# Kernel tuning notes

Hardware: AMD Instinct MI355X
Metric: run time of the kernel (lower is better)

The kernel has to match this reference:

```python
import jax, jax.numpy as jnp
import numpy as np

B, T = 4, 512
V, D, L, H, F = 32000, 1024, 12, 16, 4096
HD = D // H
CUTS = [0, 2000, 8000, V]
SHRINK = 4


def layer_norm(x, s, b, eps=1e-5):
    m = jnp.mean(x, axis=-1, keepdims=True)
    v = jnp.var(x, axis=-1, keepdims=True)
    return (x - m) * jax.lax.rsqrt(v + eps) * s + b


def rel_shift(x):
    # Transformer-XL relative shift. x: [B, H, T, S] with S == T.
    b, h, t, s = x.shape
    x = jnp.pad(x, ((0, 0), (0, 0), (0, 0), (1, 0)))
    x = x.reshape(b, h, s + 1, t)[:, :, 1:, :]
    return x.reshape(b, h, t, s)


def sinusoid_pos_emb(seq_len, dim):
    # positions seq_len-1 ... 0 (TXL convention), [seq_len, dim]
    pos = jnp.arange(seq_len - 1, -1, -1.0, dtype=jnp.float32)
    inv_freq = 1.0 / (10000.0 ** (jnp.arange(0, dim, 2, dtype=jnp.float32) / dim))
    ang = pos[:, None] * inv_freq[None, :]
    return jnp.concatenate([jnp.sin(ang), jnp.cos(ang)], axis=-1)


def setup_inputs() -> dict:
    key = jax.random.key(0)
    ks = iter(jax.random.split(key, 64))

    def n(shape, std=0.02):
        return jax.random.normal(next(ks), shape, dtype=jnp.float32) * std

    hids = [D // (SHRINK ** i) for i in range(3)]  # 1024, 256, 64
    inp = {}
    inp['x'] = jax.random.randint(next(ks), (B, T), 0, V)
    inp['emb_0'] = n([CUTS[1] - CUTS[0], hids[0]])
    inp['emb_1'] = n([CUTS[2] - CUTS[1], hids[1]])
    inp['emb_2'] = n([CUTS[3] - CUTS[2], hids[2]])
    inp['proj_1'] = n([hids[1], D], 0.01)
    inp['proj_2'] = n([hids[2], D], 0.01)
    inp['out_bias'] = jnp.zeros([V], jnp.float32)
    inp['r_w_bias'] = n([1, 1, H, HD])
    inp['r_r_bias'] = n([1, 1, H, HD])
    inp['ln1_s'] = jnp.ones([L, D], jnp.float32)
    inp['ln1_b'] = jnp.zeros([L, D], jnp.float32)
    inp['Wq'] = n([L, D, D]); inp['bq'] = jnp.zeros([L, D], jnp.float32)
    inp['Wk'] = n([L, D, D]); inp['bk'] = jnp.zeros([L, D], jnp.float32)
    inp['Wv'] = n([L, D, D]); inp['bv'] = jnp.zeros([L, D], jnp.float32)
    inp['Wr'] = n([L, D, D])  # relative position projection (no bias)
    inp['Wo'] = n([L, D, D]); inp['bo'] = jnp.zeros([L, D], jnp.float32)
    inp['ln2_s'] = jnp.ones([L, D], jnp.float32)
    inp['ln2_b'] = jnp.zeros([L, D], jnp.float32)
    inp['W1'] = n([L, D, F]); inp['b1'] = jnp.zeros([L, F], jnp.float32)
    inp['W2'] = n([L, F, D]); inp['b2'] = jnp.zeros([L, D], jnp.float32)
    return inp


def forward(x, emb_0, emb_1, emb_2, proj_1, proj_2, out_bias, r_w_bias, r_r_bias,
            ln1_s, ln1_b, Wq, bq, Wk, bk, Wv, bv, Wr, Wo, bo, ln2_s, ln2_b,
            W1, b1, W2, b2):
    Bx, Tx = x.shape
    # --- adaptive input embedding (clustered table + up-projection, scaled) ---
    embs = [emb_0, emb_1, emb_2]
    projs = [None, proj_1, proj_2]
    h = jnp.zeros((Bx, Tx, D), jnp.float32)
    for i in range(3):
        lo, hi = CUTS[i], CUTS[i + 1]
        in_bucket = (x >= lo) & (x < hi)
        idx = jnp.clip(x - lo, 0, hi - lo - 1)
        e = embs[i][idx]  # [B, T, hid_i]
        if projs[i] is not None:
            e = e @ projs[i]  # -> [B, T, D]
        h = h + jnp.where(in_bucket[..., None], e, 0.0)
    h = h * jnp.sqrt(jnp.float32(D))

    pemb = sinusoid_pos_emb(Tx, D)                  # [T, D]
    causal = jnp.tril(jnp.ones((Tx, Tx), bool))     # [T, T]
    scale = 1.0 / np.sqrt(HD)

    for i in range(L):
        # --- TXL relative-position multi-head attention (pre-norm) ---
        a_in = layer_norm(h, ln1_s[i], ln1_b[i])
        q = (a_in @ Wq[i] + bq[i]).reshape(Bx, Tx, H, HD)
        k = (a_in @ Wk[i] + bk[i]).reshape(Bx, Tx, H, HD)
        v = (a_in @ Wv[i] + bv[i]).reshape(Bx, Tx, H, HD)
        r_k = (pemb @ Wr[i]).reshape(Tx, H, HD)     # [T, H, HD]
        content = jnp.einsum('bthd,bshd->bhts', q + r_w_bias[0, 0], k)
        rel = jnp.einsum('bthd,shd->bhts', q + r_r_bias[0, 0], r_k)
        logits = (content + rel_shift(rel)) * scale
        logits = jnp.where(causal[None, None], logits, jnp.float32(-1e30))
        attn = jax.nn.softmax(logits, axis=-1)
        o = jnp.einsum('bhts,bshd->bthd', attn, v).reshape(Bx, Tx, D)
        h = h + (o @ Wo[i] + bo[i])
        # --- FFN (pre-norm, GELU) ---
        f_in = layer_norm(h, ln2_s[i], ln2_b[i])
        h = h + (jax.nn.gelu(f_in @ W1[i] + b1[i]) @ W2[i] + b2[i])

    # --- tied adaptive-softmax output projection ---
    W_full = jnp.concatenate([emb_0, emb_1 @ proj_1, emb_2 @ proj_2], axis=0)  # [V, D]
    return h @ W_full.T + out_bias  # [B, T, V]


def reference(x, emb_0, emb_1, emb_2, proj_1, proj_2, out_bias, r_w_bias, r_r_bias,
              ln1_s, ln1_b, Wq, bq, Wk, bk, Wv, bv, Wr, Wo, bo, ln2_s, ln2_b,
              W1, b1, W2, b2):
    return forward(x, emb_0, emb_1, emb_2, proj_1, proj_2, out_bias, r_w_bias,
                   r_r_bias, ln1_s, ln1_b, Wq, bq, Wk, bk, Wv, bv, Wr, Wo, bo,
                   ln2_s, ln2_b, W1, b1, W2, b2)
```

## Files before the change

### kernel.cpp

```cpp
#include <hip/hip_runtime.h>

using us = unsigned short;
typedef short short8v __attribute__((ext_vector_type(8)));
typedef float float4v __attribute__((ext_vector_type(4)));

constexpr int NB  = 4;
constexpr int NT  = 512;
constexpr int ND  = 1024;
constexpr int NL  = 12;
constexpr int NH  = 16;
constexpr int NF  = 4096;
constexpr int NHD = 64;
constexpr int NBT = NB * NT;
constexpr int NV  = 32000;
constexpr long QOFF = (long)NBT * ND;
constexpr long RKL  = 640L * 1024;

__device__ __forceinline__ us f2bf(float f) {
    unsigned u = __float_as_uint(f);
    u += 0x7fffu + ((u >> 16) & 1u);
    return (us)(u >> 16);
}

__device__ __forceinline__ void gload16(const us* g, us* l) {
    __builtin_amdgcn_global_load_lds(
        (const __attribute__((address_space(1))) void*)g,
        (__attribute__((address_space(3))) void*)l, 16, 0, 0);
}

template<int BM, int BN, int EPI, bool OUTBF>
__global__ __launch_bounds__(256)
void bgemm_k(const us* __restrict__ A, const us* __restrict__ B, void* Cv,
             const float* __restrict__ bias, const float* addsrc,
             const float* __restrict__ p0, const float* __restrict__ p1,
             us* __restrict__ vtp,
             int N, int K, int lda, int ldb, int ldc,
             int bdiv, long sAb, long sAh, long sBb, long sBh, long sCb, long sCh)
{
    constexpr int BK  = 64;
    constexpr int WTM = BM / 2, WTN = BN / 2;
    constexpr int FM  = WTM / 16, FN = WTN / 16;
    constexpr int AI  = BM / 32;
    constexpr int BI  = BN / 32;
    static_assert(BM % 32 == 0 && BN % 32 == 0, "");

    long coff = 0;
    if (bdiv > 0) {
        int z = blockIdx.z, zb = z / bdiv, zh = z % bdiv;
        A += zb * sAb + zh * sAh;
        B += zb * sBb + zh * sBh;
        coff = zb * sCb + zh * sCh;
    }
    float* Cf = (float*)Cv + coff;
    us*    Ch = (us*)Cv + coff;
    if (addsrc) addsrc += coff;

    __shared__ __align__(16) us As[BM * BK];
    __shared__ __align__(16) us Bs[BN * BK];

    const int tid  = threadIdx.x;
    const int lane = tid & 63;
    const int w    = tid >> 6;
    const int wm   = w >> 1;
    const int wn   = w & 1;
    const int row0 = blockIdx.y * BM;
    const int col0 = blockIdx.x * BN;

    float4v acc[FM][FN];
#pragma unroll
    for (int i = 0; i < FM; ++i)
#pragma unroll
        for (int j = 0; j < FN; ++j) acc[i][j] = (float4v)0.f;

    for (int k0 = 0; k0 < K; k0 += BK) {
#pragma unroll
        for (int i = 0; i < AI; ++i) {
            int rb = w * (BM / 4) + i * 8;
            int r  = rb + (lane >> 3);
            int sc8 = ((lane & 7) ^ (r & 7)) << 3;
            gload16(A + (long)(row0 + r) * lda + k0 + sc8, As + rb * 64);
        }
#pragma unroll
        for (int i = 0; i < BI; ++i) {
            int rb = w * (BN / 4) + i * 8;
            int r  = rb + (lane >> 3);
            int sc8 = ((lane & 7) ^ (r & 7)) << 3;
            gload16(B + (long)(col0 + r) * ldb + k0 + sc8, Bs + rb * 64);
        }
        __syncthreads();
#pragma unroll
        for (int ks = 0; ks < 2; ++ks) {
            short8v af[FM], bfr[FN];
            int sw = ks * 4 + (lane >> 4);
#pragma unroll
            for (int i = 0; i < FM; ++i) {
                int r = wm * WTM + i * 16 + (lane & 15);
                af[i] = *reinterpret_cast<const short8v*>((const char*)As + r * 128 + ((sw ^ (r & 7)) << 4));
            }
#pragma unroll
            for (int j = 0; j < FN; ++j) {
                int r = wn * WTN + j * 16 + (lane & 15);
                bfr[j] = *reinterpret_cast<const short8v*>((const char*)Bs + r * 128 + ((sw ^ (r & 7)) << 4));
            }
#pragma unroll
            for (int i = 0; i < FM; ++i)
#pragma unroll
                for (int j = 0; j < FN; ++j)
                    acc[i][j] = __builtin_amdgcn_mfma_f32_16x16x32_bf16(af[i], bfr[j], acc[i][j], 0, 0, 0);
        }
        __syncthreads();
    }

#pragma unroll
    for (int i = 0; i < FM; ++i) {
        int growb = row0 + wm * WTM + i * 16 + ((lane >> 4) << 2);
#pragma unroll
        for (int j = 0; j < FN; ++j) {
            int gcol = col0 + wn * WTN + j * 16 + (lane & 15);
            if (EPI == 3) {
                int seg = gcol >> 10, c = gcol & 1023;
                float bb = bias[gcol];
                if (seg == 2) {
                    unsigned lo = (unsigned)f2bf(acc[i][j][0] + bb)
                                | ((unsigned)f2bf(acc[i][j][1] + bb) << 16);
                    unsigned hi = (unsigned)f2bf(acc[i][j][2] + bb)
                                | ((unsigned)f2bf(acc[i][j][3] + bb) << 16);
                    int bidx = growb >> 9, tb = growb & 511;
                    uint2 pk; pk.x = lo; pk.y = hi;
                    *reinterpret_cast<uint2*>(
                        vtp + ((long)((bidx * 16 + (c >> 6)) * 64 + (c & 63)) << 9) + tb) = pk;
                } else {
                    us* base = (us*)Cv;
#pragma unroll
                    for (int r = 0; r < 4; ++r) {
                        int gr = growb + r;
                        float v = acc[i][j][r] + bb;
                        long o = (long)gr * 1024 + c;
                        if (seg == 0) {
                            base[o]        = f2bf(v + p0[c]);
                            base[o + QOFF] = f2bf(v + p1[c]);
                        } else base[o + 2 * QOFF] = f2bf(v);
                    }
                }
            } else {
                if (gcol >= N) continue;
#pragma unroll
                for (int r = 0; r < 4; ++r) {
                    int gr = growb + r;
                    float v = acc[i][j][r];
                    if (bias) v += bias[gcol];
                    if (EPI == 1) {
                        float xx = v;
                        v = 0.5f * xx * (1.f + tanhf(0.7978845608028654f
                                                     * (xx + 0.044715f * xx * xx * xx)));
                    }
                    if (addsrc) v += addsrc[(long)gr * ldc + gcol];
                    if (OUTBF) Ch[(long)gr * ldc + gcol] = f2bf(v);
                    else       Cf[(long)gr * ldc + gcol] = v;
                }
            }
        }
    }
}

__global__ __launch_bounds__(256)
void fattn_k(const us* __restrict__ qkv, const us* __restrict__ vt,
             const us* __restrict__ rk, us* __restrict__ obuf)
{
    __shared__ __align__(16) us lds_k[64 * 64];
    __shared__ __align__(16) us lds_v[64 * 64];
    __shared__ __align__(16) us lds_rk[64 * 64];
    __shared__ __align__(16) us lds_p[4 * 16 * 64];
    __shared__ float lds_r[4 * 16 * 132];

    const int tid = threadIdx.x, lane = tid & 63, w = tid >> 6;
    const int qt = blockIdx.x, bh = blockIdx.y;
    const int b = bh >> 4, h = bh & 15;
    const int t0 = qt * 64;
    const int rg = lane >> 4, lc = lane & 15;

    const us* qwb = qkv + ((long)b * 512) * 1024 + h * 64;
    const us* qrb = qwb + QOFF;
    const us* kb  = qwb + 2 * QOFF;
    const us* vtb = vt + (long)bh * 64 * 512;
    const us* rkb = rk + h * 64;

    short8v aqw[2], aqr[2];
    {
        long qrow = (long)(t0 + w * 16 + lc) * 1024;
        int ko = rg * 8;
        aqw[0] = *(const short8v*)(qwb + qrow + ko);
        aqw[1] = *(const short8v*)(qwb + qrow + 32 + ko);
        aqr[0] = *(const short8v*)(qrb + qrow + ko);
        aqr[1] = *(const short8v*)(qrb + qrow + 32 + ko);
    }

    float4v oacc[4];
#pragma unroll
    for (int i = 0; i < 4; ++i) oacc[i] = (float4v)0.f;
    float mrow[4] = {-3e38f, -3e38f, -3e38f, -3e38f};
    float lrow[4] = {0.f, 0.f, 0.f, 0.f};

    float* rbase = lds_r + w * (16 * 132);
    us*    pbase = lds_p + w * (16 * 64);

    auto stage_rk = [&](int j0) {
#pragma unroll
        for (int i = 0; i < 2; ++i) {
            int rb = w * 16 + i * 8;
            int r  = rb + (lane >> 3);
            int sl = ((lane & 7) ^ (r & 7)) << 3;
            gload16(rkb + (long)(j0 + r) * 1024 + sl, lds_rk + rb * 64);
        }
    };
    auto rel_half = [&](int wbase) {
#pragma unroll
        for (int jn = 0; jn < 4; ++jn) {
            float4v rf = (float4v)0.f;
#pragma unroll
            for (int kk = 0; kk < 2; ++kk) {
                int r = jn * 16 + lc;
                int sw = kk * 4 + rg;
                short8v bf = *(const short8v*)((const char*)lds_rk + r * 128 + ((sw ^ (r & 7)) << 4));
                rf = __builtin_amdgcn_mfma_f32_16x16x32_bf16(aqr[kk], bf, rf, 0, 0, 0);
            }
#pragma unroll
            for (int pr = 0; pr < 4; ++pr)
                rbase[(rg * 4 + pr) * 132 + wbase + jn * 16 + lc] = rf[pr];
        }
    };

    const int nst = qt + 1;
    for (int st = 0; st < nst; ++st) {
        const int s0 = st * 64;
        const int jb = (st - qt) * 64 + 448;
        const int sb = ((st - qt + 7) & 1) << 6;

#pragma unroll
        for (int i = 0; i < 2; ++i) {
            int rb = w * 16 + i * 8;
            int r  = rb + (lane >> 3);
            int sl = ((lane & 7) ^ (r & 7)) << 3;
            gload16(kb + (long)(s0 + r) * 1024 + sl, lds_k + rb * 64);
            gload16(vtb + (long)r * 512 + s0 + sl, lds_v + rb * 64);
        }
        if (st == 0) {
            stage_rk(jb);
            __syncthreads();
            rel_half(sb);
            __syncthreads();
            stage_rk(jb + 64);
            __syncthreads();
        } else {
            stage_rk(jb + 64);
            __syncthreads();
        }

        float4v sfr[4];
#pragma unroll
        for (int sn = 0; sn < 4; ++sn) {
            sfr[sn] = (float4v)0.f;
#pragma unroll
            for (int kk = 0; kk < 2; ++kk) {
                int r = sn * 16 + lc;
                int sw = kk * 4 + rg;
                short8v bf = *(const short8v*)((const char*)lds_k + r * 128 + ((sw ^ (r & 7)) << 4));
                sfr[sn] = __builtin_amdgcn_mfma_f32_16x16x32_bf16(aqw[kk], bf, sfr[sn], 0, 0, 0);
            }
        }
        rel_half(sb ^ 64);

        float pv[4][4];
        float rmax[4] = {-3e38f, -3e38f, -3e38f, -3e38f};
#pragma unroll
        for (int pr = 0; pr < 4; ++pr) {
            int tt = rg * 4 + pr;
            int tw = w * 16 + tt;
#pragma unroll
            for (int sn = 0; sn < 4; ++sn) {
                int ss = sn * 16 + lc;
                int slot = (sb + ss + 63 - tw) & 127;
                float lg = (sfr[sn][pr] + rbase[tt * 132 + slot]) * 0.125f;
                if (ss > t0 - s0 + tw) lg = -1e30f;
                pv[sn][pr] = lg;
                rmax[pr] = fmaxf(rmax[pr], lg);
            }
        }
#pragma unroll
        for (int o = 1; o < 16; o <<= 1)
#pragma unroll
            for (int pr = 0; pr < 4; ++pr)
                rmax[pr] = fmaxf(rmax[pr], __shfl_xor(rmax[pr], o));
        float rsum[4];
#pragma unroll
        for (int pr = 0; pr < 4; ++pr) {
            float mn = fmaxf(mrow[pr], rmax[pr]);
            float al = __expf(mrow[pr] - mn);
            mrow[pr] = mn;
            lrow[pr] *= al;
            float s = 0.f;
#pragma unroll
            for (int sn = 0; sn < 4; ++sn) {
                float p = __expf(pv[sn][pr] - mn);
                pv[sn][pr] = p;
                s += p;
            }
            rsum[pr] = s;
#pragma unroll
            for (int dn = 0; dn < 4; ++dn) oacc[dn][pr] *= al;
        }
#pragma unroll
        for (int o = 1; o < 16; o <<= 1)
#pragma unroll
            for (int pr = 0; pr < 4; ++pr)
                rsum[pr] += __shfl_xor(rsum[pr], o);
#pragma unroll
        for (int pr = 0; pr < 4; ++pr) lrow[pr] += rsum[pr];

#pragma unroll
        for (int pr = 0; pr < 4; ++pr) {
            int row = rg * 4 + pr;
#pragma unroll
            for (int sn = 0; sn < 4; ++sn) {
                int col = sn * 16 + lc;
                *(us*)((char*)pbase + row * 128 + (((col >> 3) ^ (row & 7)) << 4) + (col & 7) * 2)
                    = f2bf(pv[sn][pr]);
            }
        }
        short8v pa[2];
#pragma unroll
        for (int kk = 0; kk < 2; ++kk)
            pa[kk] = *(const short8v*)((const char*)pbase + lc * 128 + (((kk * 4 + rg) ^ (lc & 7)) << 4));
#pragma unroll
        for (int dn = 0; dn < 4; ++dn) {
#pragma unroll
            for (int kk = 0; kk < 2; ++kk) {
                int r = dn * 16 + lc;
                int sw = kk * 4 + rg;
                short8v vb = *(const short8v*)((const char*)lds_v + r * 128 + ((sw ^ (r & 7)) << 4));
                oacc[dn] = __builtin_amdgcn_mfma_f32_16x16x32_bf16(pa[kk], vb, oacc[dn], 0, 0, 0);
            }
        }
        __syncthreads();
    }
#pragma unroll
    for (int pr = 0; pr < 4; ++pr) {
        int t = t0 + w * 16 + rg * 4 + pr;
        float inv = 1.f / lrow[pr];
        long rowo = ((long)b * 512 + t) * 1024 + h * 64;
#pragma unroll
        for (int dn = 0; dn < 4; ++dn)
            obuf[rowo + dn * 16 + lc] = f2bf(oacc[dn][pr] * inv);
    }
}

__global__ __launch_bounds__(256)
void tconv_k(const float* __restrict__ in, us* __restrict__ out, int R, int C,
             long inL, long outL)
{
    in  += (long)blockIdx.z * inL;
    out += (long)blockIdx.z * outL;
    __shared__ float t[32][33];
    int c0 = blockIdx.x * 32, r0 = blockIdx.y * 32;
    int tx = threadIdx.x & 31, ty = threadIdx.x >> 5;
#pragma unroll
    for (int j = 0; j < 4; ++j)
        t[ty + j * 8][tx] = in[(long)(r0 + ty + j * 8) * C + c0 + tx];
    __syncthreads();
#pragma unroll
    for (int j = 0; j < 4; ++j)
        out[(long)(c0 + ty + j * 8) * R + r0 + tx] = f2bf(t[tx][ty + j * 8]);
}

__global__ __launch_bounds__(256)
void conv_k(const float* __restrict__ in, us* __restrict__ out, long n)
{
    long i = ((long)blockIdx.x * 256 + threadIdx.x) * 4;
    if (i >= n) return;
    float4 v = *reinterpret_cast<const float4*>(in + i);
    uint2 p;
    p.x = (unsigned)f2bf(v.x) | ((unsigned)f2bf(v.y) << 16);
    p.y = (unsigned)f2bf(v.z) | ((unsigned)f2bf(v.w) << 16);
    *reinterpret_cast<uint2*>(out + i) = p;
}

__global__ __launch_bounds__(256)
void rkpad12_k(us* __restrict__ rk)
{
    int i = blockIdx.x * 256 + threadIdx.x;
    int l = i >> 13, r = i & 8191;
    reinterpret_cast<uint4*>(rk + (long)l * RKL + 512 * 1024)[r] = make_uint4(0, 0, 0, 0);
}

__global__ __launch_bounds__(256)
void bcat_k(const float* __restrict__ bq, const float* __restrict__ bk,
            const float* __restrict__ bv, float* __restrict__ o)
{
    int i = blockIdx.x * 256 + threadIdx.x;
    int l = i / 3072, rr = i % 3072, seg = rr >> 10, c = rr & 1023;
    const float* s = seg == 0 ? bq : seg == 1 ? bk : bv;
    o[i] = s[l * 1024 + c];
}

__global__ __launch_bounds__(256)
void ln_k(const float* __restrict__ x, us* __restrict__ y,
          const float* __restrict__ sc, const float* __restrict__ bi)
{
    int row = blockIdx.x;
    const float* xr = x + (long)row * ND;
    int d4 = threadIdx.x * 4;
    float4 v = *reinterpret_cast<const float4*>(&xr[d4]);
    float sum = v.x + v.y + v.z + v.w;
    float sq  = v.x * v.x + v.y * v.y + v.z * v.z + v.w * v.w;
#pragma unroll
    for (int o = 32; o; o >>= 1) { sum += __shfl_xor(sum, o); sq += __shfl_xor(sq, o); }
    __shared__ float red[8];
    int w = threadIdx.x >> 6;
    if ((threadIdx.x & 63) == 0) { red[w] = sum; red[4 + w] = sq; }
    __syncthreads();
    sum = red[0] + red[1] + red[2] + red[3];
    sq  = red[4] + red[5] + red[6] + red[7];
    float mean = sum * (1.f / ND);
    float var  = fmaxf(sq * (1.f / ND) - mean * mean, 0.f);
    float inv  = rsqrtf(var + 1e-5f);
    float4 s4 = *reinterpret_cast<const float4*>(&sc[d4]);
    float4 b4 = *reinterpret_cast<const float4*>(&bi[d4]);
    uint2 p;
    p.x = (unsigned)f2bf((v.x - mean) * inv * s4.x + b4.x)
        | ((unsigned)f2bf((v.y - mean) * inv * s4.y + b4.y) << 16);
    p.y = (unsigned)f2bf((v.z - mean) * inv * s4.z + b4.z)
        | ((unsigned)f2bf((v.w - mean) * inv * s4.w + b4.w) << 16);
    *reinterpret_cast<uint2*>(y + (long)row * ND + d4) = p;
}

__global__ __launch_bounds__(256)
void pemb_k(us* __restrict__ p)
{
    int t = blockIdx.x;
    float pos = (float)(NT - 1 - t);
    for (int j = threadIdx.x; j < ND / 2; j += 256) {
        float invf = expf(-(float)j * (9.210340371976184f / 512.0f));
        float ang  = pos * invf;
        p[(long)t * ND + j]           = f2bf(sinf(ang));
        p[(long)t * ND + ND / 2 + j]  = f2bf(cosf(ang));
    }
}

__global__ __launch_bounds__(256)
void embed_k(const int* __restrict__ x,
             const float* __restrict__ e0, const float* __restrict__ e1,
             const float* __restrict__ e2, const float* __restrict__ p1,
             const float* __restrict__ p2, float* __restrict__ h)
{
    __shared__ float e[256];
    int tok = blockIdx.x;
    int v = x[tok];
    float* outp = h + (long)tok * ND;
    if (v < 2000) {
        const float* r = e0 + (long)v * ND;
        for (int d = threadIdx.x; d < ND; d += 256) outp[d] = r[d] * 32.0f;
    } else if (v < 8000) {
        const float* r = e1 + (long)(v - 2000) * 256;
        e[threadIdx.x] = r[threadIdx.x];
        __syncthreads();
        for (int d = threadIdx.x; d < ND; d += 256) {
            float acc = 0.f;
#pragma unroll 4
            for (int i = 0; i < 256; ++i) acc += e[i] * p1[(long)i * ND + d];
            outp[d] = acc * 32.0f;
        }
    } else {
        const float* r = e2 + (long)(v - 8000) * 64;
        if (threadIdx.x < 64) e[threadIdx.x] = r[threadIdx.x];
        __syncthreads();
        for (int d = threadIdx.x; d < ND; d += 256) {
            float acc = 0.f;
#pragma unroll 4
            for (int i = 0; i < 64; ++i) acc += e[i] * p2[(long)i * ND + d];
            outp[d] = acc * 32.0f;
        }
    }
}

extern "C" void kernel_launch(void* const* d_in, const int* in_sizes, int n_in,
                              void* d_out, int out_size, void* d_ws, size_t ws_size,
                              hipStream_t stream)
{
    (void)in_sizes; (void)n_in; (void)out_size;
    const int*   x     = (const int*)  d_in[0];
    const float* emb0  = (const float*)d_in[1];
    const float* emb1  = (const float*)d_in[2];
    const float* emb2  = (const float*)d_in[3];
    const float* proj1 = (const float*)d_in[4];
    const float* proj2 = (const float*)d_in[5];
    const float* obias = (const float*)d_in[6];
    const float* rwb   = (const float*)d_in[7];
    const float* rrb   = (const float*)d_in[8];
    const float* ln1s  = (const float*)d_in[9];
    const float* ln1b  = (const float*)d_in[10];
    const float* Wq    = (const float*)d_in[11];
    const float* bq    = (const float*)d_in[12];
    const float* Wk    = (const float*)d_in[13];
    const float* bk    = (const float*)d_in[14];
    const float* Wv    = (const float*)d_in[15];
    const float* bv    = (const float*)d_in[16];
    const float* Wr    = (const float*)d_in[17];
    const float* Wo    = (const float*)d_in[18];
    const float* bo    = (const float*)d_in[19];
    const float* ln2s  = (const float*)d_in[20];
    const float* ln2b  = (const float*)d_in[21];
    const float* W1    = (const float*)d_in[22];
    const float* b1    = (const float*)d_in[23];
    const float* W2    = (const float*)d_in[24];
    const float* b2    = (const float*)d_in[25];
    float* out = (float*)d_out;

    us* ob      = (us*)out;
    us* qkvbuf  = ob;
    us* mid_bf  = ob +  6291456;
    us* vt_bf   = ob + 14680064;
    us* o_bf    = ob + 16777216;
    us* ain_bf  = ob + 18874368;
    us* rk_all  = ob + 20971520;
    us* pemb_bf = ob + 28835840;
    us* wqkv_sc = ob + 29360128;
    us* wr_sc   = ob + 32505856;
    us* wo_sc   = ob + 33554432;
    us* w1_sc   = ob + 34603008;
    us* w2_sc   = ob + 38797312;

    float* wsf      = (float*)d_ws;
    float* h        = wsf;
    us*    h_bf     = (us*)(wsf + 2097152);
    us*    hp1_bf   = h_bf   + 2097152;
    us*    hp2_bf   = hp1_bf + 524288;
    us*    emb0_bf  = hp2_bf + 131072;
    us*    emb1_bf  = emb0_bf + 2097152;
    us*    emb2_bf  = emb1_bf + 1572864;
    us*    proj1_bf = emb2_bf + 1540096;
    us*    proj2_bf = proj1_bf + 262144;
    float* bqkv     = (float*)(proj2_bf + 65536);
    us*    wqkv_all = (us*)(bqkv + 36864);
    us*    wr_all   = wqkv_all + (long)NL * 3072 * 1024;
    us*    wo_all   = wr_all   + (long)NL * 1024 * 1024;
    us*    w1_all   = wo_all   + (long)NL * 1024 * 1024;
    us*    w2_all   = w1_all   + (long)NL * 4096 * 1024;
    const bool big  = ws_size >= (size_t)352273408;

    bcat_k<<<144, 256, 0, stream>>>(bq, bk, bv, bqkv);
    conv_k<<<2000, 256, 0, stream>>>(emb0,  emb0_bf,  2048000);
    conv_k<<<1500, 256, 0, stream>>>(emb1,  emb1_bf,  1536000);
    conv_k<<<1500, 256, 0, stream>>>(emb2,  emb2_bf,  1536000);
    conv_k<<<256,  256, 0, stream>>>(proj1, proj1_bf, 262144);
    conv_k<<<64,   256, 0, stream>>>(proj2, proj2_bf, 65536);
    pemb_k<<<NT, 256, 0, stream>>>(pemb_bf);
    rkpad12_k<<<384, 256, 0, stream>>>(rk_all);
    embed_k<<<NBT, 256, 0, stream>>>(x, emb0, emb1, emb2, proj1, proj2, h);
    if (big) {
        tconv_k<<<dim3(32, 32, NL), 256, 0, stream>>>(Wq, wqkv_all,           1024, 1024, 1048576, 3145728);
        tconv_k<<<dim3(32, 32, NL), 256, 0, stream>>>(Wk, wqkv_all + 1048576, 1024, 1024, 1048576, 3145728);
        tconv_k<<<dim3(32, 32, NL), 256, 0, stream>>>(Wv, wqkv_all + 2097152, 1024, 1024, 1048576, 3145728);
        tconv_k<<<dim3(32, 32, NL), 256, 0, stream>>>(Wr, wr_all, 1024, 1024, 1048576, 1048576);
        tconv_k<<<dim3(32, 32, NL), 256, 0, stream>>>(Wo, wo_all, 1024, 1024, 1048576, 1048576);
        tconv_k<<<dim3(128, 32, NL), 256, 0, stream>>>(W1, w1_all, 1024, 4096, 4194304, 4194304);
        tconv_k<<<dim3(32, 128, NL), 256, 0, stream>>>(W2, w2_all, 4096, 1024, 4194304, 4194304);
        bgemm_k<64, 64, 0, true><<<dim3(16, 8, NL), 256, 0, stream>>>(
            pemb_bf, wr_all, rk_all, nullptr, nullptr, nullptr, nullptr, nullptr,
            1024, 1024, 1024, 1024, 1024,
            1, 0, 0, 1048576, 0, RKL, 0);
    }

    for (int l = 0; l < NL; ++l) {
        const us* wqkv_t = big ? wqkv_all + (long)l * 3145728 : wqkv_sc;
        const us* wo_t   = big ? wo_all   + (long)l * 1048576 : wo_sc;
        const us* w1_t   = big ? w1_all   + (long)l * 4194304 : w1_sc;
        const us* w2_t   = big ? w2_all   + (long)l * 4194304 : w2_sc;
        if (!big) {
            const long wOff = (long)l * ND * ND;
            tconv_k<<<dim3(32, 32), 256, 0, stream>>>(Wq + wOff, wqkv_sc,           1024, 1024, 0, 0);
            tconv_k<<<dim3(32, 32), 256, 0, stream>>>(Wk + wOff, wqkv_sc + 1048576, 1024, 1024, 0, 0);
            tconv_k<<<dim3(32, 32), 256, 0, stream>>>(Wv + wOff, wqkv_sc + 2097152, 1024, 1024, 0, 0);
            tconv_k<<<dim3(32, 32), 256, 0, stream>>>(Wr + wOff, wr_sc, 1024, 1024, 0, 0);
            tconv_k<<<dim3(32, 32), 256, 0, stream>>>(Wo + wOff, wo_sc, 1024, 1024, 0, 0);
            tconv_k<<<dim3(128, 32), 256, 0, stream>>>(W1 + (long)l * ND * NF, w1_sc, 1024, 4096, 0, 0);
            tconv_k<<<dim3(32, 128), 256, 0, stream>>>(W2 + (long)l * ND * NF, w2_sc, 4096, 1024, 0, 0);
            bgemm_k<64, 64, 0, true><<<dim3(16, 8, 1), 256, 0, stream>>>(
                pemb_bf, wr_sc, rk_all + (long)l * RKL, nullptr, nullptr, nullptr, nullptr, nullptr,
                1024, 1024, 1024, 1024, 1024, 0, 0, 0, 0, 0, 0, 0);
        }

        ln_k<<<NBT, 256, 0, stream>>>(h, ain_bf, ln1s + l * ND, ln1b + l * ND);
        bgemm_k<128, 64, 3, true><<<dim3(48, 16, 1), 256, 0, stream>>>(
            ain_bf, wqkv_t, qkvbuf, bqkv + l * 3072, nullptr, rwb, rrb, vt_bf,
            3072, 1024, 1024, 1024, 1024, 0, 0, 0, 0, 0, 0, 0);
        fattn_k<<<dim3(8, NB * NH), 256, 0, stream>>>(
            qkvbuf, vt_bf, rk_all + (long)l * RKL, o_bf);
        bgemm_k<64, 64, 0, false><<<dim3(16, 32, 1), 256, 0, stream>>>(
            o_bf, wo_t, h, bo + l * ND, h, nullptr, nullptr, nullptr,
            1024, 1024, 1024, 1024, 1024, 0, 0, 0, 0, 0, 0, 0);

        ln_k<<<NBT, 256, 0, stream>>>(h, ain_bf, ln2s + l * ND, ln2b + l * ND);
        bgemm_k<128, 128, 1, true><<<dim3(32, 16, 1), 256, 0, stream>>>(
            ain_bf, w1_t, mid_bf, b1 + (long)l * NF, nullptr, nullptr, nullptr, nullptr,
            4096, 1024, 1024, 1024, 4096, 0, 0, 0, 0, 0, 0, 0);
        bgemm_k<64, 64, 0, false><<<dim3(16, 32, 1), 256, 0, stream>>>(
            mid_bf, w2_t, h, b2 + l * ND, h, nullptr, nullptr, nullptr,
            1024, 4096, 4096, 4096, 1024, 0, 0, 0, 0, 0, 0, 0);
    }

    conv_k<<<2048, 256, 0, stream>>>(h, h_bf, (long)NBT * ND);
    bgemm_k<128, 64, 0, false><<<dim3(32, 16, 1), 256, 0, stream>>>(
        h_bf, emb0_bf, out, obias, nullptr, nullptr, nullptr, nullptr,
        2000, 1024, 1024, 1024, NV, 0, 0, 0, 0, 0, 0, 0);
    bgemm_k<64, 64, 0, true><<<dim3(4, 32, 1), 256, 0, stream>>>(
        h_bf, proj1_bf, hp1_bf, nullptr, nullptr, nullptr, nullptr, nullptr,
        256, 1024, 1024, 1024, 256, 0, 0, 0, 0, 0, 0, 0);
    bgemm_k<128, 128, 0, false><<<dim3(47, 16, 1), 256, 0, stream>>>(
        hp1_bf, emb1_bf, out + 2000, obias + 2000, nullptr, nullptr, nullptr, nullptr,
        6000, 256, 256, 256, NV, 0, 0, 0, 0, 0, 0, 0);
    bgemm_k<64, 64, 0, true><<<dim3(1, 32, 1), 256, 0, stream>>>(
        h_bf, proj2_bf, hp2_bf, nullptr, nullptr, nullptr, nullptr, nullptr,
        64, 1024, 1024, 1024, 64, 0, 0, 0, 0, 0, 0, 0);
    bgemm_k<128, 128, 0, false><<<dim3(188, 16, 1), 256, 0, stream>>>(
        hp2_bf, emb2_bf, out + 8000, obias + 8000, nullptr, nullptr, nullptr, nullptr,
        24000, 64, 64, 64, NV, 0, 0, 0, 0, 0, 0, 0);
}
```

Before: 2.878 ms.

## Double-buffer GEMM LDS tiles and split-K the FFN down-projection with reduction kernel

The GEMM kernel now keeps two LDS buffers and issues the global loads for the next K tile before computing on the current one, dropping one barrier per iteration so memory and MFMA work can overlap. The FFN W2 GEMM (K=4096) moves from 64x64 tiles to 128x128 tiles with a 4-way split-K over blockIdx.z, writing fp32 partials into scratch space in the output buffer. A new elementwise kernel then sums the partials, adds the bias and the residual into h. This doubles LDS use per block, which may lower occupancy, and adds an extra pass over fp32 partial memory plus one more launch per layer.

New measurement: 2.572 ms. -10.7%, faster.

```diff
diff --git a/kernel.cpp b/kernel.cpp
--- a/kernel.cpp
+++ b/kernel.cpp
@@ -55,8 +55,8 @@
     us*    Ch = (us*)Cv + coff;
     if (addsrc) addsrc += coff;
 
-    __shared__ __align__(16) us As[BM * BK];
-    __shared__ __align__(16) us Bs[BN * BK];
+    __shared__ __align__(16) us As[2 * BM * BK];
+    __shared__ __align__(16) us Bs[2 * BN * BK];
 
     const int tid  = threadIdx.x;
     const int lane = tid & 63;
@@ -72,22 +72,32 @@
 #pragma unroll
         for (int j = 0; j < FN; ++j) acc[i][j] = (float4v)0.f;
 
-    for (int k0 = 0; k0 < K; k0 += BK) {
+    auto stage = [&](int buf, int k0) {
+        us* Ad = As + buf * (BM * BK);
+        us* Bd = Bs + buf * (BN * BK);
 #pragma unroll
         for (int i = 0; i < AI; ++i) {
             int rb = w * (BM / 4) + i * 8;
             int r  = rb + (lane >> 3);
             int sc8 = ((lane & 7) ^ (r & 7)) << 3;
-            gload16(A + (long)(row0 + r) * lda + k0 + sc8, As + rb * 64);
+            gload16(A + (long)(row0 + r) * lda + k0 + sc8, Ad + rb * 64);
         }
 #pragma unroll
         for (int i = 0; i < BI; ++i) {
             int rb = w * (BN / 4) + i * 8;
             int r  = rb + (lane >> 3);
             int sc8 = ((lane & 7) ^ (r & 7)) << 3;
-            gload16(B + (long)(col0 + r) * ldb + k0 + sc8, Bs + rb * 64);
-        }
-        __syncthreads();
+            gload16(B + (long)(col0 + r) * ldb + k0 + sc8, Bd + rb * 64);
+        }
+    };
+
+    stage(0, 0);
+    __syncthreads();
+    int cur = 0;
+    for (int k0 = 0; k0 < K; k0 += BK) {
+        if (k0 + BK < K) stage(cur ^ 1, k0 + BK);
+        const char* Ac = (const char*)(As + cur * (BM * BK));
+        const char* Bc = (const char*)(Bs + cur * (BN * BK));
 #pragma unroll
         for (int ks = 0; ks < 2; ++ks) {
             short8v af[FM], bfr[FN];
@@ -95,12 +105,12 @@
 #pragma unroll
             for (int i = 0; i < FM; ++i) {
                 int r = wm * WTM + i * 16 + (lane & 15);
-                af[i] = *reinterpret_cast<const short8v*>((const char*)As + r * 128 + ((sw ^ (r & 7)) << 4));
+                af[i] = *reinterpret_cast<const short8v*>(Ac + r * 128 + ((sw ^ (r & 7)) << 4));
             }
 #pragma unroll
             for (int j = 0; j < FN; ++j) {
                 int r = wn * WTN + j * 16 + (lane & 15);
-                bfr[j] = *reinterpret_cast<const short8v*>((const char*)Bs + r * 128 + ((sw ^ (r & 7)) << 4));
+                bfr[j] = *reinterpret_cast<const short8v*>(Bc + r * 128 + ((sw ^ (r & 7)) << 4));
             }
 #pragma unroll
             for (int i = 0; i < FM; ++i)
@@ -109,6 +119,7 @@
                     acc[i][j] = __builtin_amdgcn_mfma_f32_16x16x32_bf16(af[i], bfr[j], acc[i][j], 0, 0, 0);
         }
         __syncthreads();
+        cur ^= 1;
     }
 
 #pragma unroll
@@ -161,6 +172,24 @@
             }
         }
     }
+}
+
+__global__ __launch_bounds__(256)
+void ffnred_k(const float* __restrict__ part, const float* __restrict__ b2v,
+              float* __restrict__ h)
+{
+    long i = ((long)blockIdx.x * 256 + threadIdx.x) * 4;
+    float4 a0 = *reinterpret_cast<const float4*>(part + i);
+    float4 a1 = *reinterpret_cast<const float4*>(part + i + 2097152);
+    float4 a2 = *reinterpret_cast<const float4*>(part + i + 4194304);
+    float4 a3 = *reinterpret_cast<const float4*>(part + i + 6291456);
+    float4 hv = *reinterpret_cast<const float4*>(h + i);
+    float4 bb = *reinterpret_cast<const float4*>(b2v + (int)(i & 1023));
+    hv.x += a0.x + a1.x + a2.x + a3.x + bb.x;
+    hv.y += a0.y + a1.y + a2.y + a3.y + bb.y;
+    hv.z += a0.z + a1.z + a2.z + a3.z + bb.z;
+    hv.w += a0.w + a1.w + a2.w + a3.w + bb.w;
+    *reinterpret_cast<float4*>(h + i) = hv;
 }
 
 __global__ __launch_bounds__(256)
@@ -528,6 +557,7 @@
     us* wo_sc   = ob + 33554432;
     us* w1_sc   = ob + 34603008;
     us* w2_sc   = ob + 38797312;
+    float* pffn = out + 21495808;
 
     float* wsf      = (float*)d_ws;
     float* h        = wsf;
@@ -603,9 +633,11 @@
         bgemm_k<128, 128, 1, true><<<dim3(32, 16, 1), 256, 0, stream>>>(
             ain_bf, w1_t, mid_bf, b1 + (long)l * NF, nullptr, nullptr, nullptr, nullptr,
             4096, 1024, 1024, 1024, 4096, 0, 0, 0, 0, 0, 0, 0);
-        bgemm_k<64, 64, 0, false><<<dim3(16, 32, 1), 256, 0, stream>>>(
-            mid_bf, w2_t, h, b2 + l * ND, h, nullptr, nullptr, nullptr,
-            1024, 4096, 4096, 4096, 1024, 0, 0, 0, 0, 0, 0, 0);
+        bgemm_k<128, 128, 0, false><<<dim3(8, 16, 4), 256, 0, stream>>>(
+            mid_bf, w2_t, pffn, nullptr, nullptr, nullptr, nullptr, nullptr,
+            1024, 1024, 4096, 4096, 1024,
+            1, 1024, 0, 1024, 0, 2097152, 0);
+        ffnred_k<<<2048, 256, 0, stream>>>(pffn, b2 + (long)l * ND, h);
     }
 
     conv_k<<<2048, 256, 0, stream>>>(h, h_bf, (long)NBT * ND);
```
